# Kernel tuning notes

Hardware: AMD Instinct MI355X
Metric: run time of the kernel (lower is better)

Reference implementation:

```python
import jax, jax.numpy as jnp
import numpy as np

RF = 3          # receptive_field_size (cubic)
STRIDE = 1
TEMP = 1.0      # softmax temperature ('soft' sampling, eval mode: no Gumbel noise)
TREE_DEPTH = 4

# Truth table of all 16 binary gates: GATES[g, t] = value of gate g on input
# pattern t = 2*a + b (a = first child, b = second child), t in {0,1,2,3}.
GATES = np.array([[(g >> t) & 1 for t in range(4)] for g in range(16)],
                 dtype=np.float32)  # (16, 4)


def _lut_eval(a, b, w):
    """Differentiable 2-input LUT. a, b: (B,K,P,nodes); w: (nodes,K,16)."""
    probs = jax.nn.softmax(w / TEMP, axis=-1)          # (nodes,K,16)
    lut = probs @ jnp.asarray(GATES)                   # (nodes,K,4) relaxed truth table
    lut = jnp.moveaxis(lut, 0, 1)[:, None]             # (K,1,nodes,4) -> bcast over B,P
    l0, l1, l2, l3 = lut[..., 0], lut[..., 1], lut[..., 2], lut[..., 3]
    na, nb = 1.0 - a, 1.0 - b
    # E[lut(a,b)] under independent Bernoulli inputs
    return l0 * na * nb + l1 * na * b + l2 * a * nb + l3 * a * b


def setup_inputs() -> dict:
    key = jax.random.key(0)
    ks = jax.random.split(key, 8)
    B, C, H, W, D = 4, 3, 32, 32, 32
    K, S = 32, 16  # num_kernels, lut_rank**tree_depth leaves
    x = jax.random.uniform(ks[0], (B, C, H, W, D), dtype=jnp.float32)
    # (lut_rank=2, K, S, 4) coords (h, w, d, c); rf=3 and channels=3 so all in [0,3)
    kernel_coords = jax.random.randint(ks[1], (2, K, S, 4), 0, 3, dtype=jnp.int32)
    w0 = jax.random.normal(ks[2], (16, K, 16), dtype=jnp.float32)
    w1 = jax.random.normal(ks[3], (8, K, 16), dtype=jnp.float32)
    w2 = jax.random.normal(ks[4], (4, K, 16), dtype=jnp.float32)
    w3 = jax.random.normal(ks[5], (2, K, 16), dtype=jnp.float32)
    w4 = jax.random.normal(ks[6], (1, K, 16), dtype=jnp.float32)
    return {"x": x, "kernel_coords": kernel_coords,
            "w0": w0, "w1": w1, "w2": w2, "w3": w3, "w4": w4}


def reference(x, kernel_coords, w0, w1, w2, w3, w4):
    B, C, H, W, D = x.shape
    OH, OW, OD = (H - RF) // STRIDE + 1, (W - RF) // STRIDE + 1, (D - RF) // STRIDE + 1
    kc = kernel_coords
    # linear offset of each leaf coord inside flattened (C,H,W,D) volume
    base = ((kc[..., 3] * H + kc[..., 0]) * W + kc[..., 1]) * D + kc[..., 2]  # (2,K,S)
    oh = jnp.arange(OH) * STRIDE
    ow = jnp.arange(OW) * STRIDE
    od = jnp.arange(OD) * STRIDE
    patch = ((oh[:, None, None] * W + ow[None, :, None]) * D
             + od[None, None, :]).reshape(-1)                                  # (P,)
    lin = base[:, :, None, :] + patch[None, None, :, None]                     # (2,K,P,S)
    g = x.reshape(B, -1)[:, lin]                                               # (B,2,K,P,S)
    out = _lut_eval(g[:, 0], g[:, 1], w0)                                      # (B,K,P,S)
    for w in (w1, w2, w3, w4):  # binary tree reduction over TREE_DEPTH levels
        out = _lut_eval(out[..., 0::2], out[..., 1::2], w)
    return out.reshape(B, out.shape[1], OH, OW, OD)
```

## Files before the change

### kernel.cpp

```cpp
#include <hip/hip_runtime.h>


#define B_  4
#define C_  3
#define H_  32
#define W_  32
#define D_  32
#define K_  32
#define S_  16
#define WS  33
#define TPB 512

typedef float v8f __attribute__((ext_vector_type(8), aligned(4)));

__device__ __forceinline__ v8f lut8(v8f a, v8f b, float l0, float d1, float d2, float d3) {
    const v8f t0 = a * d2 + l0;
    const v8f t1 = a * d3 + d1;
    return b * t1 + t0;
}

__global__ __launch_bounds__(TPB, 4) void logic_conv3d(
    const float* __restrict__ x,
    const int*   __restrict__ kc,
    const float* __restrict__ w0,
    const float* __restrict__ w1,
    const float* __restrict__ w2,
    const float* __restrict__ w3,
    const float* __restrict__ w4,
    float*       __restrict__ out)
{
    __shared__ float4 s_lut[2][31];
    __shared__ __align__(16) int s_lb[2][16];
    __shared__ __align__(16) int s_gb[2][16];
    __shared__ __align__(16) float slab[18 * 32 * WS];

    const int bx  = blockIdx.x;
    const int b   = bx >> 4;
    const int k0  = (bx & 15) << 1;
    const int tid = threadIdx.x;
    const int oh0 = blockIdx.y * 4;

    if (tid < 62) {
        const int kk   = (tid >= 31) ? 1 : 0;
        const int node = tid - kk * 31;
        const int k    = k0 + kk;
        const float* wp; int ln;
        if      (node < 16) { wp = w0; ln = node;      }
        else if (node < 24) { wp = w1; ln = node - 16; }
        else if (node < 28) { wp = w2; ln = node - 24; }
        else if (node < 30) { wp = w3; ln = node - 28; }
        else                { wp = w4; ln = 0;         }
        const float* wrow = wp + (ln * K_ + k) * 16;
        float lg[16];
        float m = -1e30f;
        #pragma unroll
        for (int g = 0; g < 16; ++g) { lg[g] = wrow[g]; m = fmaxf(m, lg[g]); }
        float z = 0.f;
        #pragma unroll
        for (int g = 0; g < 16; ++g) { lg[g] = __expf(lg[g] - m); z += lg[g]; }
        const float inv = 1.0f / z;
        float l0 = 0.f, l1 = 0.f, l2 = 0.f, l3 = 0.f;
        #pragma unroll
        for (int g = 0; g < 16; ++g) {
            float p = lg[g] * inv;
            if (g & 1) l0 += p;
            if (g & 2) l1 += p;
            if (g & 4) l2 += p;
            if (g & 8) l3 += p;
        }
        s_lut[kk][node] = make_float4(l0, l1 - l0, l2 - l0, (l3 - l2) - (l1 - l0));
    } else if (tid >= 64 && tid < 128) {
        const int idx  = tid - 64;
        const int kk   = idx >> 5;
        const int tree = (idx >> 4) & 1;
        const int s    = idx & 15;
        const int k    = k0 + kk;
        const int off  = ((tree * K_ + k) * S_ + s) * 4;
        const int h = kc[off + 0], w = kc[off + 1], d = kc[off + 2], c = kc[off + 3];
        if (tree == 0)
            s_lb[kk][s] = ((c * 6 + h) * 32 + w) * WS + d;
        else
            s_gb[kk][s] = ((c * H_ + h) * W_ + w) * D_ + d;
    }

    {
        const float* xb = x + (size_t)b * (C_ * H_ * W_ * D_);
        #pragma unroll
        for (int it = 0; it < 9; ++it) {
            const int idx   = it * TPB + tid;
            const int plane = idx >> 8;
            const int f4    = idx & 255;
            const int c     = plane / 6;
            const int dh    = plane - c * 6;
            const int h     = min(oh0 + dh, H_ - 1);
            const int w     = f4 >> 3;
            const int d4    = (f4 & 7) << 2;
            const float4 val = *(const float4*)(xb + ((c * H_ + h) * W_ + w) * D_ + d4);
            *(float4*)&slab[(plane * 32 + w) * WS + d4] = val;
        }
    }
    __syncthreads();

    int sA[2][16], sB[2][16];
    #pragma unroll
    for (int kk = 0; kk < 2; ++kk) {
        #pragma unroll
        for (int i = 0; i < 4; ++i) {
            const int4 qa = *(const int4*)&s_lb[kk][i * 4];
            sA[kk][i * 4 + 0] = __builtin_amdgcn_readfirstlane(qa.x);
            sA[kk][i * 4 + 1] = __builtin_amdgcn_readfirstlane(qa.y);
            sA[kk][i * 4 + 2] = __builtin_amdgcn_readfirstlane(qa.z);
            sA[kk][i * 4 + 3] = __builtin_amdgcn_readfirstlane(qa.w);
            const int4 qb = *(const int4*)&s_gb[kk][i * 4];
            sB[kk][i * 4 + 0] = __builtin_amdgcn_readfirstlane(qb.x);
            sB[kk][i * 4 + 1] = __builtin_amdgcn_readfirstlane(qb.y);
            sB[kk][i * 4 + 2] = __builtin_amdgcn_readfirstlane(qb.z);
            sB[kk][i * 4 + 3] = __builtin_amdgcn_readfirstlane(qb.w);
        }
    }

    const int ohl = tid >> 7;
    const int r   = tid & 127;
    const int ow  = r >> 2;
    const int gq  = r & 3;
    const int od0 = (gq < 3) ? (gq << 3) : 22;
    const int oh  = oh0 + ohl;

    if (ow < 30 && oh < 30) {
        const int vo  = ohl * (32 * WS) + ow * WS + od0;
        const int gvo = ohl * (W_ * D_) + ow * D_ + od0;
        const float* xg = x + (size_t)b * (C_ * H_ * W_ * D_) + oh0 * (W_ * D_);

        #define LD_A(kk, s) (*(const v8f*)&slab[sA[kk][s] + vo])
        #define LD_B(kk, s) (*(const v8f*)(xg + sB[kk][s] + gvo))

        v8f cA0 = LD_A(0, 0), cB0 = LD_B(0, 0);
        v8f cA1 = LD_A(0, 1), cB1 = LD_B(0, 1);

        v8f v1[8];
        #pragma unroll
        for (int kk = 0; kk < 2; ++kk) {
            #pragma unroll
            for (int j = 0; j < 8; ++j) {
                const int nkk = (j == 7) ? kk + 1 : kk;
                const int nj  = (j == 7) ? 0 : j + 1;
                v8f nA0 = cA0, nB0 = cB0, nA1 = cA1, nB1 = cB1;
                if (nkk < 2) {
                    nB0 = LD_B(nkk, 2 * nj);
                    nB1 = LD_B(nkk, 2 * nj + 1);
                    nA0 = LD_A(nkk, 2 * nj);
                    nA1 = LD_A(nkk, 2 * nj + 1);
                }
                const float4 L0 = s_lut[kk][2 * j];
                const v8f t0 = lut8(cA0, cB0, L0.x, L0.y, L0.z, L0.w);
                const float4 L1 = s_lut[kk][2 * j + 1];
                const v8f t1 = lut8(cA1, cB1, L1.x, L1.y, L1.z, L1.w);
                const float4 LN = s_lut[kk][16 + j];
                v1[j] = lut8(t0, t1, LN.x, LN.y, LN.z, LN.w);
                cA0 = nA0; cB0 = nB0; cA1 = nA1; cB1 = nB1;
            }

            v8f v2[4];
            #pragma unroll
            for (int j = 0; j < 4; ++j) {
                const float4 L = s_lut[kk][24 + j];
                v2[j] = lut8(v1[2 * j], v1[2 * j + 1], L.x, L.y, L.z, L.w);
            }
            v8f v3[2];
            #pragma unroll
            for (int j = 0; j < 2; ++j) {
                const float4 L = s_lut[kk][28 + j];
                v3[j] = lut8(v2[2 * j], v2[2 * j + 1], L.x, L.y, L.z, L.w);
            }
            v8f v4;
            {
                const float4 L = s_lut[kk][30];
                v4 = lut8(v3[0], v3[1], L.x, L.y, L.z, L.w);
            }

            const int bk = b * K_ + k0 + kk;
            float* outp = out + (size_t)bk * 27000 + oh * 900 + ow * 30 + od0;
            *(v8f*)outp = v4;
        }
        #undef LD_A
        #undef LD_B
    }
}

extern "C" void kernel_launch(void* const* d_in, const int* in_sizes, int n_in,
                              void* d_out, int out_size, void* d_ws, size_t ws_size,
                              hipStream_t stream) {
    const float* x  = (const float*)d_in[0];
    const int*   kc = (const int*)d_in[1];
    const float* w0 = (const float*)d_in[2];
    const float* w1 = (const float*)d_in[3];
    const float* w2 = (const float*)d_in[4];
    const float* w3 = (const float*)d_in[5];
    const float* w4 = (const float*)d_in[6];
    float* out = (float*)d_out;

    dim3 grid((B_ * K_) / 2, 8);
    logic_conv3d<<<grid, TPB, 0, stream>>>(x, kc, w0, w1, w2, w3, w4, out);
}
```

Measured before the change: 81.42 us.

## Read both gather trees from LDS slab and interleave per-wave kernel order

Second-tree leaf gathers now read from the shared-memory slab instead of global memory, since the slab already covers the needed rows. The explicit software prefetch pipeline is replaced by a depth-first tree evaluation, which lowers register pressure. Alternating waves process the two kernels in opposite order, which may spread LDS bank and output-store traffic. The cost is more LDS reads per thread and reliance on the compiler to schedule the loads.

```diff
diff --git a/kernel.cpp b/kernel.cpp
--- a/kernel.cpp
+++ b/kernel.cpp
@@ -77,10 +77,9 @@
         const int k    = k0 + kk;
         const int off  = ((tree * K_ + k) * S_ + s) * 4;
         const int h = kc[off + 0], w = kc[off + 1], d = kc[off + 2], c = kc[off + 3];
-        if (tree == 0)
-            s_lb[kk][s] = ((c * 6 + h) * 32 + w) * WS + d;
-        else
-            s_gb[kk][s] = ((c * H_ + h) * W_ + w) * D_ + d;
+        const int sb = ((c * 6 + h) * 32 + w) * WS + d;
+        if (tree == 0) s_lb[kk][s] = sb;
+        else           s_gb[kk][s] = sb;
     }
 
     {
@@ -127,63 +126,51 @@
     const int oh  = oh0 + ohl;
 
     if (ow < 30 && oh < 30) {
-        const int vo  = ohl * (32 * WS) + ow * WS + od0;
-        const int gvo = ohl * (W_ * D_) + ow * D_ + od0;
-        const float* xg = x + (size_t)b * (C_ * H_ * W_ * D_) + oh0 * (W_ * D_);
+        const int vo = ohl * (32 * WS) + ow * WS + od0;
 
-        #define LD_A(kk, s) (*(const v8f*)&slab[sA[kk][s] + vo])
-        #define LD_B(kk, s) (*(const v8f*)(xg + sB[kk][s] + gvo))
+        #define LD_T0(kk, s) (*(const v8f*)&slab[sA[kk][s] + vo])
+        #define LD_T1(kk, s) (*(const v8f*)&slab[sB[kk][s] + vo])
 
-        v8f cA0 = LD_A(0, 0), cB0 = LD_B(0, 0);
-        v8f cA1 = LD_A(0, 1), cB1 = LD_B(0, 1);
+        #define KK_BODY(kk) do {                                                  \
+            v8f v2[4];                                                            \
+            _Pragma("unroll")                                                     \
+            for (int q = 0; q < 4; ++q) {                                         \
+                v8f tl[2];                                                        \
+                _Pragma("unroll")                                                 \
+                for (int u = 0; u < 2; ++u) {                                     \
+                    const int j = 2 * q + u;                                      \
+                    const v8f A0 = LD_T0(kk, 2 * j);                              \
+                    const v8f B0 = LD_T1(kk, 2 * j);                              \
+                    const float4 L0 = s_lut[kk][2 * j];                           \
+                    const v8f t0 = lut8(A0, B0, L0.x, L0.y, L0.z, L0.w);          \
+                    const v8f A1 = LD_T0(kk, 2 * j + 1);                          \
+                    const v8f B1 = LD_T1(kk, 2 * j + 1);                          \
+                    const float4 L1 = s_lut[kk][2 * j + 1];                       \
+                    const v8f t1 = lut8(A1, B1, L1.x, L1.y, L1.z, L1.w);          \
+                    const float4 LN = s_lut[kk][16 + j];                          \
+                    tl[u] = lut8(t0, t1, LN.x, LN.y, LN.z, LN.w);                 \
+                }                                                                 \
+                const float4 L2 = s_lut[kk][24 + q];                              \
+                v2[q] = lut8(tl[0], tl[1], L2.x, L2.y, L2.z, L2.w);               \
+            }                                                                     \
+            const float4 La = s_lut[kk][28];                                      \
+            const v8f u0 = lut8(v2[0], v2[1], La.x, La.y, La.z, La.w);            \
+            const float4 Lb = s_lut[kk][29];                                      \
+            const v8f u1 = lut8(v2[2], v2[3], Lb.x, Lb.y, Lb.z, Lb.w);            \
+            const float4 Lc = s_lut[kk][30];                                      \
+            const v8f u2 = lut8(u0, u1, Lc.x, Lc.y, Lc.z, Lc.w);                  \
+            const int bk = b * K_ + k0 + (kk);                                    \
+            float* outp = out + (size_t)bk * 27000 + oh * 900 + ow * 30 + od0;    \
+            *(v8f*)outp = u2;                                                     \
+        } while (0)
 
-        v8f v1[8];
-        #pragma unroll
-        for (int kk = 0; kk < 2; ++kk) {
-            #pragma unroll
-            for (int j = 0; j < 8; ++j) {
-                const int nkk = (j == 7) ? kk + 1 : kk;
-                const int nj  = (j == 7) ? 0 : j + 1;
-                v8f nA0 = cA0, nB0 = cB0, nA1 = cA1, nB1 = cB1;
-                if (nkk < 2) {
-                    nB0 = LD_B(nkk, 2 * nj);
-                    nB1 = LD_B(nkk, 2 * nj + 1);
-                    nA0 = LD_A(nkk, 2 * nj);
-                    nA1 = LD_A(nkk, 2 * nj + 1);
-                }
-                const float4 L0 = s_lut[kk][2 * j];
-                const v8f t0 = lut8(cA0, cB0, L0.x, L0.y, L0.z, L0.w);
-                const float4 L1 = s_lut[kk][2 * j + 1];
-                const v8f t1 = lut8(cA1, cB1, L1.x, L1.y, L1.z, L1.w);
-                const float4 LN = s_lut[kk][16 + j];
-                v1[j] = lut8(t0, t1, LN.x, LN.y, LN.z, LN.w);
-                cA0 = nA0; cB0 = nB0; cA1 = nA1; cB1 = nB1;
-            }
+        const int wpar = (tid >> 6) & 1;
+        if (wpar == 0) { KK_BODY(0); KK_BODY(1); }
+        else           { KK_BODY(1); KK_BODY(0); }
 
-            v8f v2[4];
-            #pragma unroll
-            for (int j = 0; j < 4; ++j) {
-                const float4 L = s_lut[kk][24 + j];
-                v2[j] = lut8(v1[2 * j], v1[2 * j + 1], L.x, L.y, L.z, L.w);
-            }
-            v8f v3[2];
-            #pragma unroll
-            for (int j = 0; j < 2; ++j) {
-                const float4 L = s_lut[kk][28 + j];
-                v3[j] = lut8(v2[2 * j], v2[2 * j + 1], L.x, L.y, L.z, L.w);
-            }
-            v8f v4;
-            {
-                const float4 L = s_lut[kk][30];
-                v4 = lut8(v3[0], v3[1], L.x, L.y, L.z, L.w);
-            }
-
-            const int bk = b * K_ + k0 + kk;
-            float* outp = out + (size_t)bk * 27000 + oh * 900 + ow * 30 + od0;
-            *(v8f*)outp = v4;
-        }
-        #undef LD_A
-        #undef LD_B
+        #undef KK_BODY
+        #undef LD_T0
+        #undef LD_T1
     }
 }
 
```

New measurement: 86.94 us. 1.07x slower.

## Switch to one output row per block with scalar per-thread outputs

Applied to the files above, without the earlier changes.

Restructures the tiling so each block handles a single output height row instead of four. The shared-memory slab shrinks to 3 planes per channel, and the grid grows from 8 to 30 rows. Each thread now computes scalar outputs along the depth axis rather than 8-wide vectors, and occupancy hints rise to 8 blocks per CU. The aim is more parallelism and occupancy with lower register pressure, at the cost of more redundant slab loads, more LUT prologue work per output, and narrower global loads and stores.

```diff
diff --git a/kernel.cpp b/kernel.cpp
--- a/kernel.cpp
+++ b/kernel.cpp
@@ -8,18 +8,13 @@
 #define D_  32
 #define K_  32
 #define S_  16
-#define WS  33
 #define TPB 512
 
-typedef float v8f __attribute__((ext_vector_type(8), aligned(4)));
-
-__device__ __forceinline__ v8f lut8(v8f a, v8f b, float l0, float d1, float d2, float d3) {
-    const v8f t0 = a * d2 + l0;
-    const v8f t1 = a * d3 + d1;
-    return b * t1 + t0;
+__device__ __forceinline__ float lut1(float a, float b, float l0, float d1, float d2, float d3) {
+    return fmaf(b, fmaf(a, d3, d1), fmaf(a, d2, l0));
 }
 
-__global__ __launch_bounds__(TPB, 4) void logic_conv3d(
+__global__ __launch_bounds__(TPB, 8) void logic_conv3d(
     const float* __restrict__ x,
     const int*   __restrict__ kc,
     const float* __restrict__ w0,
@@ -32,13 +27,13 @@
     __shared__ float4 s_lut[2][31];
     __shared__ __align__(16) int s_lb[2][16];
     __shared__ __align__(16) int s_gb[2][16];
-    __shared__ __align__(16) float slab[18 * 32 * WS];
+    __shared__ __align__(16) float slab[3 * 3 * 32 * 32];
 
     const int bx  = blockIdx.x;
     const int b   = bx >> 4;
     const int k0  = (bx & 15) << 1;
     const int tid = threadIdx.x;
-    const int oh0 = blockIdx.y * 4;
+    const int oh  = blockIdx.y;
 
     if (tid < 62) {
         const int kk   = (tid >= 31) ? 1 : 0;
@@ -78,25 +73,27 @@
         const int off  = ((tree * K_ + k) * S_ + s) * 4;
         const int h = kc[off + 0], w = kc[off + 1], d = kc[off + 2], c = kc[off + 3];
         if (tree == 0)
-            s_lb[kk][s] = ((c * 6 + h) * 32 + w) * WS + d;
+            s_lb[kk][s] = ((c * 3 + h) * 32 + w) * 32 + d;
         else
-            s_gb[kk][s] = ((c * H_ + h) * W_ + w) * D_ + d;
+            s_gb[kk][s] = ((c * H_ + (oh + h)) * W_ + w) * D_ + d;
     }
 
+    const float* xg = x + (size_t)b * (C_ * H_ * W_ * D_);
+
     {
-        const float* xb = x + (size_t)b * (C_ * H_ * W_ * D_);
         #pragma unroll
-        for (int it = 0; it < 9; ++it) {
-            const int idx   = it * TPB + tid;
-            const int plane = idx >> 8;
-            const int f4    = idx & 255;
-            const int c     = plane / 6;
-            const int dh    = plane - c * 6;
-            const int h     = min(oh0 + dh, H_ - 1);
-            const int w     = f4 >> 3;
-            const int d4    = (f4 & 7) << 2;
-            const float4 val = *(const float4*)(xb + ((c * H_ + h) * W_ + w) * D_ + d4);
-            *(float4*)&slab[(plane * 32 + w) * WS + d4] = val;
+        for (int it = 0; it < 5; ++it) {
+            const int idx = it * TPB + tid;
+            if (it < 4 || idx < 2304) {
+                const int plane = idx >> 8;
+                const int f4    = idx & 255;
+                const int c     = plane / 3;
+                const int hh    = plane - c * 3;
+                const int w     = f4 >> 3;
+                const int d4    = (f4 & 7) << 2;
+                const float4 val = *(const float4*)(xg + ((c * H_ + (oh + hh)) * W_ + w) * D_ + d4);
+                *(float4*)&slab[((c * 3 + hh) * 32 + w) * 32 + d4] = val;
+            }
         }
     }
     __syncthreads();
@@ -119,71 +116,53 @@
         }
     }
 
-    const int ohl = tid >> 7;
-    const int r   = tid & 127;
-    const int ow  = r >> 2;
-    const int gq  = r & 3;
-    const int od0 = (gq < 3) ? (gq << 3) : 22;
-    const int oh  = oh0 + ohl;
+    const int odr = tid & 31;
+    const int odc = min(odr, 29);
+    const int col = tid >> 5;
 
-    if (ow < 30 && oh < 30) {
-        const int vo  = ohl * (32 * WS) + ow * WS + od0;
-        const int gvo = ohl * (W_ * D_) + ow * D_ + od0;
-        const float* xg = x + (size_t)b * (C_ * H_ * W_ * D_) + oh0 * (W_ * D_);
+    #pragma unroll
+    for (int p = 0; p < 2; ++p) {
+        const int ow = col + p * 16;
+        if (ow < 30) {
+            const int lt = ow * 32 + odc;
 
-        #define LD_A(kk, s) (*(const v8f*)&slab[sA[kk][s] + vo])
-        #define LD_B(kk, s) (*(const v8f*)(xg + sB[kk][s] + gvo))
+            #pragma unroll
+            for (int kk = 0; kk < 2; ++kk) {
+                float v1[8];
+                #pragma unroll
+                for (int j = 0; j < 8; ++j) {
+                    const int s0 = 2 * j, s1 = 2 * j + 1;
+                    const float a0 = slab[sA[kk][s0] + lt];
+                    const float b0 = xg[sB[kk][s0] + lt];
+                    const float4 L0 = s_lut[kk][s0];
+                    const float t0 = lut1(a0, b0, L0.x, L0.y, L0.z, L0.w);
+                    const float a1 = slab[sA[kk][s1] + lt];
+                    const float b1 = xg[sB[kk][s1] + lt];
+                    const float4 L1 = s_lut[kk][s1];
+                    const float t1 = lut1(a1, b1, L1.x, L1.y, L1.z, L1.w);
+                    const float4 LN = s_lut[kk][16 + j];
+                    v1[j] = lut1(t0, t1, LN.x, LN.y, LN.z, LN.w);
+                }
 
-        v8f cA0 = LD_A(0, 0), cB0 = LD_B(0, 0);
-        v8f cA1 = LD_A(0, 1), cB1 = LD_B(0, 1);
+                #pragma unroll
+                for (int j = 0; j < 4; ++j) {
+                    const float4 L = s_lut[kk][24 + j];
+                    v1[j] = lut1(v1[2 * j], v1[2 * j + 1], L.x, L.y, L.z, L.w);
+                }
+                #pragma unroll
+                for (int j = 0; j < 2; ++j) {
+                    const float4 L = s_lut[kk][28 + j];
+                    v1[j] = lut1(v1[2 * j], v1[2 * j + 1], L.x, L.y, L.z, L.w);
+                }
+                const float4 LT = s_lut[kk][30];
+                const float r = lut1(v1[0], v1[1], LT.x, LT.y, LT.z, LT.w);
 
-        v8f v1[8];
-        #pragma unroll
-        for (int kk = 0; kk < 2; ++kk) {
-            #pragma unroll
-            for (int j = 0; j < 8; ++j) {
-                const int nkk = (j == 7) ? kk + 1 : kk;
-                const int nj  = (j == 7) ? 0 : j + 1;
-                v8f nA0 = cA0, nB0 = cB0, nA1 = cA1, nB1 = cB1;
-                if (nkk < 2) {
-                    nB0 = LD_B(nkk, 2 * nj);
-                    nB1 = LD_B(nkk, 2 * nj + 1);
-                    nA0 = LD_A(nkk, 2 * nj);
-                    nA1 = LD_A(nkk, 2 * nj + 1);
+                if (odr < 30) {
+                    const int bk = b * K_ + k0 + kk;
+                    out[(size_t)bk * 27000 + oh * 900 + ow * 30 + odr] = r;
                 }
-                const float4 L0 = s_lut[kk][2 * j];
-                const v8f t0 = lut8(cA0, cB0, L0.x, L0.y, L0.z, L0.w);
-                const float4 L1 = s_lut[kk][2 * j + 1];
-                const v8f t1 = lut8(cA1, cB1, L1.x, L1.y, L1.z, L1.w);
-                const float4 LN = s_lut[kk][16 + j];
-                v1[j] = lut8(t0, t1, LN.x, LN.y, LN.z, LN.w);
-                cA0 = nA0; cB0 = nB0; cA1 = nA1; cB1 = nB1;
             }
-
-            v8f v2[4];
-            #pragma unroll
-            for (int j = 0; j < 4; ++j) {
-                const float4 L = s_lut[kk][24 + j];
-                v2[j] = lut8(v1[2 * j], v1[2 * j + 1], L.x, L.y, L.z, L.w);
-            }
-            v8f v3[2];
-            #pragma unroll
-            for (int j = 0; j < 2; ++j) {
-                const float4 L = s_lut[kk][28 + j];
-                v3[j] = lut8(v2[2 * j], v2[2 * j + 1], L.x, L.y, L.z, L.w);
-            }
-            v8f v4;
-            {
-                const float4 L = s_lut[kk][30];
-                v4 = lut8(v3[0], v3[1], L.x, L.y, L.z, L.w);
-            }
-
-            const int bk = b * K_ + k0 + kk;
-            float* outp = out + (size_t)bk * 27000 + oh * 900 + ow * 30 + od0;
-            *(v8f*)outp = v4;
         }
-        #undef LD_A
-        #undef LD_B
     }
 }
 
@@ -199,6 +178,6 @@
     const float* w4 = (const float*)d_in[6];
     float* out = (float*)d_out;
 
-    dim3 grid((B_ * K_) / 2, 8);
+    dim3 grid(B_ * K_ / 2, 30);
     logic_conv3d<<<grid, TPB, 0, stream>>>(x, kc, w0, w1, w2, w3, w4, out);
 }
```

Result: slower. 92.36 us (+13.4%).
